# Kernel tuning notes

Hardware: AMD Instinct MI355X
Metric: run time of the kernel (lower is better)

The kernel has to match this reference:

```python
import jax, jax.numpy as jnp
import numpy as np

B, S, D, H = 4, 2048, 1024, 16  # batch, seq, n_embd, n_head
HD = D // H  # head size = 64


def setup_inputs() -> dict:
    key = jax.random.key(0)
    ks = jax.random.split(key, 5)
    s = 0.02
    return {
        "x": jax.random.normal(ks[0], (B, S, D), dtype=jnp.float32),
        "W_attn": jax.random.normal(ks[1], (D, 3 * D), dtype=jnp.float32) * s,
        "b_attn": jnp.zeros((3 * D,), dtype=jnp.float32),
        "W_proj": jax.random.normal(ks[2], (D, D), dtype=jnp.float32) * s,
        "b_proj": jnp.zeros((D,), dtype=jnp.float32),
    }


def reference(x, W_attn, b_attn, W_proj, b_proj):
    Bx, Sx, Dx = x.shape
    qkv = x @ W_attn + b_attn  # [B,S,3D]
    q, k, v = jnp.split(qkv, 3, axis=-1)
    # [B,H,S,hd]
    q = q.reshape(Bx, Sx, H, HD).transpose(0, 2, 1, 3)
    k = k.reshape(Bx, Sx, H, HD).transpose(0, 2, 1, 3)
    v = v.reshape(Bx, Sx, H, HD).transpose(0, 2, 1, 3)
    scale = 1.0 / jnp.sqrt(jnp.asarray(HD, dtype=x.dtype))
    att = jnp.einsum("bhqd,bhkd->bhqk", q, k) * scale  # [B,H,S,S]
    causal = jnp.tril(jnp.ones((Sx, Sx), dtype=bool))
    att = jnp.where(causal[None, None, :, :], att, jnp.asarray(-jnp.inf, dtype=att.dtype))
    att = jax.nn.softmax(att, axis=-1)
    y = jnp.einsum("bhqk,bhkd->bhqd", att, v)  # [B,H,S,hd]
    y = y.transpose(0, 2, 1, 3).reshape(Bx, Sx, Dx)
    return y @ W_proj + b_proj
```

## Files before the change

### kernel.cpp

```cpp
#include <hip/hip_runtime.h>
#include <math.h>

#define SEQ 2048
#define DIM 1024
#define NH 16
#define HD 64
#define QKV_LD 3072

typedef __attribute__((ext_vector_type(8))) __bf16 bf16x8;
typedef __attribute__((ext_vector_type(8))) unsigned short u16x8;
typedef __attribute__((ext_vector_type(4))) unsigned short u16x4;
typedef __attribute__((ext_vector_type(4))) float f32x4;

typedef unsigned int __attribute__((may_alias)) u32a;

__device__ __forceinline__ unsigned short f2b(float f) {
  unsigned int b = __builtin_bit_cast(unsigned int, f);
  return (unsigned short)((b + 0x7fffu + ((b >> 16) & 1u)) >> 16);
}

__device__ __forceinline__ void gload_lds16(const void* g, void* l) {
  __builtin_amdgcn_global_load_lds((const __attribute__((address_space(1))) void*)g,
                                   (__attribute__((address_space(3))) void*)l,
                                   16, 0, 0);
}

__device__ __forceinline__ bf16x8 ld_frag16(const unsigned short* p) {
  bf16x8 r;
  __builtin_memcpy(&r, __builtin_assume_aligned((void*)p, 16), 16);
  return r;
}


__global__ void to_bf16_kernel(const float* __restrict__ x,
                               unsigned short* __restrict__ y, int n) {
  int i = (blockIdx.x * blockDim.x + threadIdx.x) * 4;
  if (i >= n) return;
  float4 v = *(const float4*)(x + i);
  u16x4 o;
  o.x = f2b(v.x); o.y = f2b(v.y); o.z = f2b(v.z); o.w = f2b(v.w);
  *(u16x4*)(y + i) = o;
}

__global__ void transpose_to_bf16_kernel(const float* __restrict__ W,
                                         unsigned short* __restrict__ WT,
                                         int K, int N) {
  __shared__ float tile[32][33];
  const int n0 = blockIdx.x * 32, k0 = blockIdx.y * 32;
  const int tx = threadIdx.x, ty = threadIdx.y;
  tile[ty][tx] = W[(size_t)(k0 + ty) * N + n0 + tx];
  __syncthreads();
  WT[(size_t)(n0 + ty) * K + k0 + tx] = f2b(tile[tx][ty]);
}


template <int OUT_F32>
__global__ __launch_bounds__(256, 2) void gemm_bt_kernel(
    const unsigned short* __restrict__ A,
    const unsigned short* __restrict__ BT,
    const float* __restrict__ bias,
    void* __restrict__ C, int M, int N, int K,
    int scale_cols, float scale_val) {
  __shared__ unsigned short As[128 * 32];
  __shared__ unsigned short Bs[128 * 32];

  const int tid = threadIdx.x;
  const int wave = tid >> 6;
  const int lane = tid & 63;
  const int quad = lane >> 4;
  const int l16 = lane & 15;
  const int m0 = blockIdx.y * 128;
  const int n0 = blockIdx.x * 128;
  const int wm = (wave >> 1) * 64;
  const int wn = (wave & 1) * 64;

  const size_t a_g = (size_t)(m0 + wave * 32 + (lane >> 2)) * K + (lane & 3) * 8;
  const size_t b_g = (size_t)(n0 + wave * 32 + (lane >> 2)) * K + (lane & 3) * 8;
  unsigned short* lA = As + wave * 1024;
  unsigned short* lB = Bs + wave * 1024;

  f32x4 acc[4][4] = {};

  for (int k0 = 0; k0 < K; k0 += 32) {
    gload_lds16(A + a_g + k0, lA);
    gload_lds16(A + a_g + (size_t)16 * K + k0, lA + 512);
    gload_lds16(BT + b_g + k0, lB);
    gload_lds16(BT + b_g + (size_t)16 * K + k0, lB + 512);
    __syncthreads();

    bf16x8 af[4], bfr[4];
#pragma unroll
    for (int i = 0; i < 4; ++i)
      af[i] = *(const bf16x8*)&As[(wm + i * 16 + l16) * 32 + quad * 8];
#pragma unroll
    for (int i = 0; i < 4; ++i)
      bfr[i] = *(const bf16x8*)&Bs[(wn + i * 16 + l16) * 32 + quad * 8];
#pragma unroll
    for (int mi = 0; mi < 4; ++mi)
#pragma unroll
      for (int ni = 0; ni < 4; ++ni)
        acc[mi][ni] = __builtin_amdgcn_mfma_f32_16x16x32_bf16(af[mi], bfr[ni],
                                                              acc[mi][ni], 0, 0, 0);
    __syncthreads();
  }

#pragma unroll
  for (int mi = 0; mi < 4; ++mi) {
#pragma unroll
    for (int ni = 0; ni < 4; ++ni) {
      const int col = n0 + wn + ni * 16 + l16;
      const int row = m0 + wm + mi * 16 + quad * 4;
      const float bv = bias[col];
      const float sv = (col < scale_cols) ? scale_val : 1.0f;
#pragma unroll
      for (int r = 0; r < 4; ++r) {
        float v = (acc[mi][ni][r] + bv) * sv;
        if (OUT_F32)
          ((float*)C)[(size_t)(row + r) * N + col] = v;
        else
          ((unsigned short*)C)[(size_t)(row + r) * N + col] = f2b(v);
      }
    }
  }
}


__global__ __launch_bounds__(256, 4) void flash_kernel(
    const unsigned short* __restrict__ qkv,
    unsigned short* __restrict__ yatt) {
  __shared__ unsigned short Ks[2][2][64 * 32];
  __shared__ __align__(16) unsigned short Vt[8 * 64 * 8];
  __shared__ __align__(16) unsigned short Ps[4][16 * 72];

  const int tid = threadIdx.x;
  const int w = tid >> 6;
  const int lane = tid & 63;
  const int quad = lane >> 4;
  const int l16 = lane & 15;
  const int b = blockIdx.y >> 4;
  const int h = blockIdx.y & 15;
  const int jt = blockIdx.x;

  const unsigned short* base = qkv + (size_t)b * SEQ * QKV_LD;

  const int ktok_l = w * 16 + (lane >> 2);
  const int ksw = (ktok_l ^ (ktok_l >> 2)) & 3;
  const int kchunk = (lane & 3) ^ ksw;
  const int rsw = (l16 ^ (l16 >> 2)) & 3;

  const int vk = tid >> 3;
  const int vc = (tid & 7) * 8;

  int vwidx[8];
#pragma unroll
  for (int j = 0; j < 8; ++j)
    vwidx[j] = (vk >> 2) * 256 + (vc | ((j + (vc >> 3)) & 7)) * 4 + (vk & 3);

  int vroff[4];
#pragma unroll
  for (int ni = 0; ni < 4; ++ni) {
    const int dim = ni * 16 + l16;
    vroff[ni] = ((dim & 56) | ((dim + (dim >> 3)) & 7)) * 8;
  }

  u16x8 ob = {};
  if (l16 == 0) {
#pragma unroll
    for (int j = 0; j < 8; ++j) ob[j] = 0x3F80;
  }
  const bf16x8 onesb = __builtin_bit_cast(bf16x8, ob);

  for (int pass = 0; pass < 2; ++pass) {
    const int qt = pass == 0 ? (31 - jt) : jt;
    const int q0 = qt * 64;
    const int kt = qt + 1;

    const unsigned short* qp =
        base + (size_t)(q0 + w * 16 + l16) * QKV_LD + h * HD + quad * 8;
    const bf16x8 qf0 = *(const bf16x8*)qp;
    const bf16x8 qf1 = *(const bf16x8*)(qp + 32);

    f32x4 o[4] = {};
    f32x4 lacc = {};

    u16x8 va, vb;
    {
      const unsigned short* kg =
          base + (size_t)ktok_l * QKV_LD + DIM + h * HD + kchunk * 8;
      gload_lds16(kg, &Ks[0][0][w * 512]);
      gload_lds16(kg + 32, &Ks[0][1][w * 512]);
      const unsigned short* vg =
          base + (size_t)(2 * vk) * QKV_LD + 2 * DIM + h * HD + vc;
      va = *(const u16x8*)vg;
      vb = *(const u16x8*)(vg + QKV_LD);
    }
    __syncthreads();
    {
      u32a* V32 = (u32a*)Vt;
#pragma unroll
      for (int j = 0; j < 8; ++j)
        V32[vwidx[j]] = (unsigned int)va[j] | ((unsigned int)vb[j] << 16);
    }
    __syncthreads();

    for (int t = 0; t < kt; ++t) {
      const int cur = t & 1;
      if (t + 1 < kt) {
        const unsigned short* kg =
            base + (size_t)((t + 1) * 64 + ktok_l) * QKV_LD + DIM + h * HD + kchunk * 8;
        gload_lds16(kg, &Ks[1 - cur][0][w * 512]);
        gload_lds16(kg + 32, &Ks[1 - cur][1][w * 512]);
        const unsigned short* vg =
            base + (size_t)((t + 1) * 64 + 2 * vk) * QKV_LD + 2 * DIM + h * HD + vc;
        va = *(const u16x8*)vg;
        vb = *(const u16x8*)(vg + QKV_LD);
      }

      const bool diag = (t == kt - 1);
      const int qloc = w * 16 + quad * 4;
#pragma unroll
      for (int ni = 0; ni < 4; ++ni) {
        const int ro = (ni * 16 + l16) * 32 + ((quad ^ rsw) * 8);
        f32x4 a = {};
        a = __builtin_amdgcn_mfma_f32_16x16x32_bf16(
            qf0, *(const bf16x8*)&Ks[cur][0][ro], a, 0, 0, 0);
        a = __builtin_amdgcn_mfma_f32_16x16x32_bf16(
            qf1, *(const bf16x8*)&Ks[cur][1][ro], a, 0, 0, 0);
        const int kloc = ni * 16 + l16;
#pragma unroll
        for (int r = 0; r < 4; ++r) {
          float p = exp2f(a[r]);
          if (diag && kloc > qloc + r) p = 0.0f;
          Ps[w][(quad * 4 + r) * 72 + kloc] = f2b(p);
        }
      }

#pragma unroll
      for (int c = 0; c < 2; ++c) {
        const bf16x8 pa = ld_frag16(&Ps[w][l16 * 72 + c * 32 + quad * 8]);
#pragma unroll
        for (int ni = 0; ni < 4; ++ni) {
          const bf16x8 vbf = *(const bf16x8*)&Vt[(c * 4 + quad) * 512 + vroff[ni]];
          o[ni] = __builtin_amdgcn_mfma_f32_16x16x32_bf16(pa, vbf, o[ni], 0, 0, 0);
        }
        lacc = __builtin_amdgcn_mfma_f32_16x16x32_bf16(pa, onesb, lacc, 0, 0, 0);
      }

      __syncthreads();
      if (t + 1 < kt) {
        u32a* V32 = (u32a*)Vt;
#pragma unroll
        for (int j = 0; j < 8; ++j)
          V32[vwidx[j]] = (unsigned int)va[j] | ((unsigned int)vb[j] << 16);
      }
      __syncthreads();
    }

#pragma unroll
    for (int r = 0; r < 4; ++r) {
      const float lv = __shfl(lacc[r], quad << 4);
      const float inv = 1.0f / lv;
      const int row = q0 + w * 16 + quad * 4 + r;
      unsigned short* dst = yatt + (size_t)(b * SEQ + row) * DIM + h * HD + l16;
#pragma unroll
      for (int ni = 0; ni < 4; ++ni)
        dst[ni * 16] = f2b(o[ni][r] * inv);
    }
  }
}


extern "C" void kernel_launch(void* const* d_in, const int* in_sizes, int n_in,
                              void* d_out, int out_size, void* d_ws, size_t ws_size,
                              hipStream_t stream) {
  const float* x  = (const float*)d_in[0];
  const float* Wa = (const float*)d_in[1];
  const float* ba = (const float*)d_in[2];
  const float* Wp = (const float*)d_in[3];
  const float* bp = (const float*)d_in[4];
  float* out = (float*)d_out;

  char* ws = (char*)d_ws;
  unsigned short* xb   = (unsigned short*)ws;
  unsigned short* WaT  = (unsigned short*)(ws + 16777216);
  unsigned short* WpT  = (unsigned short*)(ws + 23068672);
  unsigned short* qkv  = (unsigned short*)(ws + 25165824);
  unsigned short* yatt = (unsigned short*)(ws + 75497472);

  const int M = 4 * SEQ;
  const float qscale = 0.125f * 1.44269504089f;

  to_bf16_kernel<<<8192, 256, 0, stream>>>(x, xb, M * DIM);
  transpose_to_bf16_kernel<<<dim3(96, 32), dim3(32, 32), 0, stream>>>(Wa, WaT, DIM, 3 * DIM);
  transpose_to_bf16_kernel<<<dim3(32, 32), dim3(32, 32), 0, stream>>>(Wp, WpT, DIM, DIM);

  gemm_bt_kernel<0><<<dim3(24, 64), 256, 0, stream>>>(xb, WaT, ba, qkv, M, 3 * DIM, DIM,
                                                      DIM, qscale);

  flash_kernel<<<dim3(16, 4 * NH), 256, 0, stream>>>(qkv, yatt);

  gemm_bt_kernel<1><<<dim3(8, 64), 256, 0, stream>>>(yatt, WpT, bp, out, M, DIM, DIM,
                                                     0, 1.0f);
}
```

Measured before the change: 283.4 us.

## Process two 64-row query tiles per flash block to reuse K/V tiles

The flash kernel now handles a 128-row query block split into two 64-row sub-tiles per pass. Each staged K/V tile is loaded into registers once and reused for both sub-tiles, with causal skipping of the upper sub-tile on the last key tile. The aim is to halve K/V global and LDS traffic per query row. In exchange it doubles accumulator registers, lowers the occupancy target to 2, and halves the grid to 512 blocks, which may hurt latency hiding and load balance.

Measured after the change: 289.9 us. 2.3% more time.

```diff
diff --git a/kernel.cpp b/kernel.cpp
--- a/kernel.cpp
+++ b/kernel.cpp
@@ -125,7 +125,7 @@
 }
 
 
-__global__ __launch_bounds__(256, 4) void flash_kernel(
+__global__ __launch_bounds__(256, 2) void flash_kernel(
     const unsigned short* __restrict__ qkv,
     unsigned short* __restrict__ yatt) {
   __shared__ unsigned short Ks[2][2][64 * 32];
@@ -171,17 +171,21 @@
   const bf16x8 onesb = __builtin_bit_cast(bf16x8, ob);
 
   for (int pass = 0; pass < 2; ++pass) {
-    const int qt = pass == 0 ? (31 - jt) : jt;
-    const int q0 = qt * 64;
-    const int kt = qt + 1;
-
-    const unsigned short* qp =
-        base + (size_t)(q0 + w * 16 + l16) * QKV_LD + h * HD + quad * 8;
-    const bf16x8 qf0 = *(const bf16x8*)qp;
-    const bf16x8 qf1 = *(const bf16x8*)(qp + 32);
-
-    f32x4 o[4] = {};
-    f32x4 lacc = {};
+    const int qt = pass == 0 ? (15 - jt) : jt;
+    const int q0 = qt * 128;
+    const int kt = 2 * qt + 2;
+
+    bf16x8 qf[2][2];
+#pragma unroll
+    for (int m = 0; m < 2; ++m) {
+      const unsigned short* qp =
+          base + (size_t)(q0 + m * 64 + w * 16 + l16) * QKV_LD + h * HD + quad * 8;
+      qf[m][0] = *(const bf16x8*)qp;
+      qf[m][1] = *(const bf16x8*)(qp + 32);
+    }
+
+    f32x4 o[2][4] = {};
+    f32x4 lacc[2] = {};
 
     u16x8 va, vb;
     {
@@ -216,34 +220,48 @@
         vb = *(const u16x8*)(vg + QKV_LD);
       }
 
-      const bool diag = (t == kt - 1);
-      const int qloc = w * 16 + quad * 4;
+      bf16x8 kf[2][4], vf[2][4];
 #pragma unroll
       for (int ni = 0; ni < 4; ++ni) {
         const int ro = (ni * 16 + l16) * 32 + ((quad ^ rsw) * 8);
-        f32x4 a = {};
-        a = __builtin_amdgcn_mfma_f32_16x16x32_bf16(
-            qf0, *(const bf16x8*)&Ks[cur][0][ro], a, 0, 0, 0);
-        a = __builtin_amdgcn_mfma_f32_16x16x32_bf16(
-            qf1, *(const bf16x8*)&Ks[cur][1][ro], a, 0, 0, 0);
-        const int kloc = ni * 16 + l16;
-#pragma unroll
-        for (int r = 0; r < 4; ++r) {
-          float p = exp2f(a[r]);
-          if (diag && kloc > qloc + r) p = 0.0f;
-          Ps[w][(quad * 4 + r) * 72 + kloc] = f2b(p);
+        kf[0][ni] = ld_frag16(&Ks[cur][0][ro]);
+        kf[1][ni] = ld_frag16(&Ks[cur][1][ro]);
+      }
+#pragma unroll
+      for (int c = 0; c < 2; ++c)
+#pragma unroll
+        for (int ni = 0; ni < 4; ++ni)
+          vf[c][ni] = ld_frag16(&Vt[(c * 4 + quad) * 512 + vroff[ni]]);
+
+      const int qloc = w * 16 + quad * 4;
+#pragma unroll
+      for (int m = 0; m < 2; ++m) {
+        if (m == 0 && t == kt - 1) continue;
+        const bool diag = (t == kt - 2 + m);
+
+#pragma unroll
+        for (int ni = 0; ni < 4; ++ni) {
+          f32x4 a = {};
+          a = __builtin_amdgcn_mfma_f32_16x16x32_bf16(qf[m][0], kf[0][ni], a, 0, 0, 0);
+          a = __builtin_amdgcn_mfma_f32_16x16x32_bf16(qf[m][1], kf[1][ni], a, 0, 0, 0);
+          const int kloc = ni * 16 + l16;
+#pragma unroll
+          for (int r = 0; r < 4; ++r) {
+            float p = exp2f(a[r]);
+            if (diag && kloc > qloc + r) p = 0.0f;
+            Ps[w][(quad * 4 + r) * 72 + kloc] = f2b(p);
+          }
         }
-      }
-
-#pragma unroll
-      for (int c = 0; c < 2; ++c) {
-        const bf16x8 pa = ld_frag16(&Ps[w][l16 * 72 + c * 32 + quad * 8]);
-#pragma unroll
-        for (int ni = 0; ni < 4; ++ni) {
-          const bf16x8 vbf = *(const bf16x8*)&Vt[(c * 4 + quad) * 512 + vroff[ni]];
-          o[ni] = __builtin_amdgcn_mfma_f32_16x16x32_bf16(pa, vbf, o[ni], 0, 0, 0);
+
+#pragma unroll
+        for (int c = 0; c < 2; ++c) {
+          const bf16x8 pa = ld_frag16(&Ps[w][l16 * 72 + c * 32 + quad * 8]);
+#pragma unroll
+          for (int ni = 0; ni < 4; ++ni)
+            o[m][ni] = __builtin_amdgcn_mfma_f32_16x16x32_bf16(pa, vf[c][ni],
+                                                               o[m][ni], 0, 0, 0);
+          lacc[m] = __builtin_amdgcn_mfma_f32_16x16x32_bf16(pa, onesb, lacc[m], 0, 0, 0);
         }
-        lacc = __builtin_amdgcn_mfma_f32_16x16x32_bf16(pa, onesb, lacc, 0, 0, 0);
       }
 
       __syncthreads();
@@ -257,14 +275,17 @@
     }
 
 #pragma unroll
-    for (int r = 0; r < 4; ++r) {
-      const float lv = __shfl(lacc[r], quad << 4);
-      const float inv = 1.0f / lv;
-      const int row = q0 + w * 16 + quad * 4 + r;
-      unsigned short* dst = yatt + (size_t)(b * SEQ + row) * DIM + h * HD + l16;
-#pragma unroll
-      for (int ni = 0; ni < 4; ++ni)
-        dst[ni * 16] = f2b(o[ni][r] * inv);
+    for (int m = 0; m < 2; ++m) {
+#pragma unroll
+      for (int r = 0; r < 4; ++r) {
+        const float lv = __shfl(lacc[m][r], quad << 4);
+        const float inv = 1.0f / lv;
+        const int row = q0 + m * 64 + w * 16 + quad * 4 + r;
+        unsigned short* dst = yatt + (size_t)(b * SEQ + row) * DIM + h * HD + l16;
+#pragma unroll
+        for (int ni = 0; ni < 4; ++ni)
+          dst[ni * 16] = f2b(o[m][ni][r] * inv);
+      }
     }
   }
 }
@@ -297,7 +318,7 @@
   gemm_bt_kernel<0><<<dim3(24, 64), 256, 0, stream>>>(xb, WaT, ba, qkv, M, 3 * DIM, DIM,
                                                       DIM, qscale);
 
-  flash_kernel<<<dim3(16, 4 * NH), 256, 0, stream>>>(qkv, yatt);
+  flash_kernel<<<dim3(8, 4 * NH), 256, 0, stream>>>(qkv, yatt);
 
   gemm_bt_kernel<1><<<dim3(8, 64), 256, 0, stream>>>(yatt, WpT, bp, out, M, DIM, DIM,
                                                      0, 1.0f);
```

## Process 128-row query blocks per K/V tile with triple-buffered continuous pipeline

Applied to the files above, without the earlier changes.

The flash kernel now gives each wave two 64-row query sub-blocks (128 rows per workgroup), so every loaded K/V tile is reused for twice as many queries. The two paired query tiles run as one continuous stream of 34 K/V tiles with a 3-deep K ring buffer, prefetch two tiles ahead, and hand-written waitcnt+barrier asm in place of __syncthreads. The grid is halved to 8x64 workgroups, launch bounds drop to 2 blocks per CU, and P is rounded to bf16 by truncation instead of round-to-nearest. In exchange it uses more registers, has fewer workgroups for load balance, and the hand-tuned vmcnt assumptions are fragile.

Result: no change. 282.4 us (-0.3%).

```diff
diff --git a/kernel.cpp b/kernel.cpp
--- a/kernel.cpp
+++ b/kernel.cpp
@@ -30,6 +30,10 @@
   __builtin_memcpy(&r, __builtin_assume_aligned((void*)p, 16), 16);
   return r;
 }
+
+#define BARRIER_VM4()  asm volatile("s_waitcnt vmcnt(4)\ns_barrier" ::: "memory")
+#define BARRIER_LGKM() asm volatile("s_waitcnt lgkmcnt(0)\ns_barrier" ::: "memory")
+#define ISSUE_FENCE()  asm volatile("" ::: "memory")
 
 
 __global__ void to_bf16_kernel(const float* __restrict__ x,
@@ -125,10 +129,93 @@
 }
 
 
-__global__ __launch_bounds__(256, 4) void flash_kernel(
+#define FA_PREFETCH(g_, via_, vib_)                                            \
+  {                                                                            \
+    const int _g = (g_);                                                       \
+    const int _tg = (_g < ktA) ? _g : ((_g < 34) ? (_g - ktA) : 0);            \
+    const unsigned short* _kg =                                                \
+        base + (size_t)(_tg * 64 + ktok_l) * QKV_LD + DIM + h * HD + kchunk * 8; \
+    gload_lds16(_kg, &Ks[_g % 3][0][w * 512]);                                 \
+    gload_lds16(_kg + 32, &Ks[_g % 3][1][w * 512]);                            \
+    const unsigned short* _vg =                                                \
+        base + (size_t)(_tg * 64 + 2 * vk) * QKV_LD + 2 * DIM + h * HD + vc;   \
+    via_ = *(const u16x8*)_vg;                                                 \
+    vib_ = *(const u16x8*)(_vg + QKV_LD);                                      \
+  }
+
+#define VT_WRITE(va_, vb_)                                                     \
+  {                                                                            \
+    u32a* _V32 = (u32a*)Vt;                                                    \
+    _Pragma("unroll") for (int j = 0; j < 8; ++j)                              \
+      _V32[vwidx[j]] = (unsigned int)(va_)[j] | ((unsigned int)(vb_)[j] << 16);\
+  }
+
+#define FA_COMPUTE(i_, t_, kt_, qf_)                                           \
+  {                                                                            \
+    const unsigned short* _kb0 = &Ks[(i_) % 3][0][0];                          \
+    const unsigned short* _kb1 = &Ks[(i_) % 3][1][0];                          \
+    bf16x8 kf0[4], kf1[4], vf0[4], vf1[4];                                     \
+    _Pragma("unroll") for (int ni = 0; ni < 4; ++ni) {                         \
+      const int ro = (ni * 16 + l16) * 32 + ((quad ^ rsw) * 8);                \
+      kf0[ni] = ld_frag16(_kb0 + ro);                                          \
+      kf1[ni] = ld_frag16(_kb1 + ro);                                          \
+      vf0[ni] = ld_frag16(&Vt[quad * 512 + vroff[ni]]);                        \
+      vf1[ni] = ld_frag16(&Vt[(4 + quad) * 512 + vroff[ni]]);                  \
+    }                                                                          \
+    const int qloc = w * 16 + quad * 4;                                        \
+    _Pragma("unroll") for (int m = 0; m < 2; ++m) {                            \
+      if (!(m == 0 && (t_) == (kt_)-1)) {   \
+        const bool diag = ((t_) == (kt_)-2 + m);                               \
+        _Pragma("unroll") for (int ni = 0; ni < 4; ++ni) {                     \
+          f32x4 a = {};                                                        \
+          a = __builtin_amdgcn_mfma_f32_16x16x32_bf16(qf_[m][0], kf0[ni], a, 0, 0, 0); \
+          a = __builtin_amdgcn_mfma_f32_16x16x32_bf16(qf_[m][1], kf1[ni], a, 0, 0, 0); \
+          const int kloc = ni * 16 + l16;                                      \
+          _Pragma("unroll") for (int r = 0; r < 4; ++r) {                      \
+            float p = exp2f(a[r]);                                             \
+            if (diag && kloc > qloc + r) p = 0.0f;                 \
+            Ps[w][(quad * 4 + r) * 72 + kloc] =                                \
+                (unsigned short)(__builtin_bit_cast(unsigned int, p) >> 16);   \
+          }                                                                    \
+        }                                                                      \
+        _Pragma("unroll") for (int c = 0; c < 2; ++c) {                        \
+          const bf16x8 pa = ld_frag16(&Ps[w][l16 * 72 + c * 32 + quad * 8]);   \
+          _Pragma("unroll") for (int ni = 0; ni < 4; ++ni)                     \
+            o[m][ni] = __builtin_amdgcn_mfma_f32_16x16x32_bf16(                \
+                pa, c ? vf1[ni] : vf0[ni], o[m][ni], 0, 0, 0);                 \
+          lacc[m] = __builtin_amdgcn_mfma_f32_16x16x32_bf16(pa, onesb,         \
+                                                            lacc[m], 0, 0, 0);\
+        }                                                                      \
+      }                                                                        \
+    }                                                                          \
+  }
+
+#define FA_ITER(i_, t_, kt_, qf_, pva, pvb, cva, cvb)                          \
+  {                                                                            \
+    FA_PREFETCH((i_) + 2, pva, pvb);                                           \
+    FA_COMPUTE(i_, t_, kt_, qf_);                                              \
+    BARRIER_VM4();                                                             \
+    if ((i_) + 1 < 34) {                                                       \
+      VT_WRITE(cva, cvb);                                                      \
+      BARRIER_LGKM();                                                          \
+    }                                                                          \
+  }
+
+#define FA_EPILOGUE(q0_)                                                       \
+  _Pragma("unroll") for (int m = 0; m < 2; ++m)                                \
+  _Pragma("unroll") for (int r = 0; r < 4; ++r) {                              \
+    const float lv = __shfl(lacc[m][r], quad << 4);                            \
+    const float inv = 1.0f / lv;                                               \
+    const int row = (q0_) + m * 64 + w * 16 + quad * 4 + r;                    \
+    unsigned short* dst = yatt + (size_t)(b * SEQ + row) * DIM + h * HD + l16; \
+    _Pragma("unroll") for (int ni = 0; ni < 4; ++ni)                           \
+      dst[ni * 16] = f2b(o[m][ni][r] * inv);                                   \
+  }
+
+__global__ __launch_bounds__(256, 2) void flash_kernel(
     const unsigned short* __restrict__ qkv,
     unsigned short* __restrict__ yatt) {
-  __shared__ unsigned short Ks[2][2][64 * 32];
+  __shared__ unsigned short Ks[3][2][64 * 32];
   __shared__ __align__(16) unsigned short Vt[8 * 64 * 8];
   __shared__ __align__(16) unsigned short Ps[4][16 * 72];
 
@@ -143,6 +230,11 @@
 
   const unsigned short* base = qkv + (size_t)b * SEQ * QKV_LD;
 
+  const int qtA = 15 - jt, qtB = jt;
+  const int ktA = 2 * qtA + 2;
+  const int ktB = 34 - ktA;
+  const int q0A = qtA * 128, q0B = qtB * 128;
+
   const int ktok_l = w * 16 + (lane >> 2);
   const int ksw = (ktok_l ^ (ktok_l >> 2)) & 3;
   const int kchunk = (lane & 3) ^ ksw;
@@ -150,12 +242,10 @@
 
   const int vk = tid >> 3;
   const int vc = (tid & 7) * 8;
-
   int vwidx[8];
 #pragma unroll
   for (int j = 0; j < 8; ++j)
     vwidx[j] = (vk >> 2) * 256 + (vc | ((j + (vc >> 3)) & 7)) * 4 + (vk & 3);
-
   int vroff[4];
 #pragma unroll
   for (int ni = 0; ni < 4; ++ni) {
@@ -170,103 +260,48 @@
   }
   const bf16x8 onesb = __builtin_bit_cast(bf16x8, ob);
 
-  for (int pass = 0; pass < 2; ++pass) {
-    const int qt = pass == 0 ? (31 - jt) : jt;
-    const int q0 = qt * 64;
-    const int kt = qt + 1;
-
-    const unsigned short* qp =
-        base + (size_t)(q0 + w * 16 + l16) * QKV_LD + h * HD + quad * 8;
-    const bf16x8 qf0 = *(const bf16x8*)qp;
-    const bf16x8 qf1 = *(const bf16x8*)(qp + 32);
-
-    f32x4 o[4] = {};
-    f32x4 lacc = {};
-
-    u16x8 va, vb;
-    {
-      const unsigned short* kg =
-          base + (size_t)ktok_l * QKV_LD + DIM + h * HD + kchunk * 8;
-      gload_lds16(kg, &Ks[0][0][w * 512]);
-      gload_lds16(kg + 32, &Ks[0][1][w * 512]);
-      const unsigned short* vg =
-          base + (size_t)(2 * vk) * QKV_LD + 2 * DIM + h * HD + vc;
-      va = *(const u16x8*)vg;
-      vb = *(const u16x8*)(vg + QKV_LD);
-    }
-    __syncthreads();
-    {
-      u32a* V32 = (u32a*)Vt;
-#pragma unroll
-      for (int j = 0; j < 8; ++j)
-        V32[vwidx[j]] = (unsigned int)va[j] | ((unsigned int)vb[j] << 16);
-    }
-    __syncthreads();
-
-    for (int t = 0; t < kt; ++t) {
-      const int cur = t & 1;
-      if (t + 1 < kt) {
-        const unsigned short* kg =
-            base + (size_t)((t + 1) * 64 + ktok_l) * QKV_LD + DIM + h * HD + kchunk * 8;
-        gload_lds16(kg, &Ks[1 - cur][0][w * 512]);
-        gload_lds16(kg + 32, &Ks[1 - cur][1][w * 512]);
-        const unsigned short* vg =
-            base + (size_t)((t + 1) * 64 + 2 * vk) * QKV_LD + 2 * DIM + h * HD + vc;
-        va = *(const u16x8*)vg;
-        vb = *(const u16x8*)(vg + QKV_LD);
-      }
-
-      const bool diag = (t == kt - 1);
-      const int qloc = w * 16 + quad * 4;
-#pragma unroll
-      for (int ni = 0; ni < 4; ++ni) {
-        const int ro = (ni * 16 + l16) * 32 + ((quad ^ rsw) * 8);
-        f32x4 a = {};
-        a = __builtin_amdgcn_mfma_f32_16x16x32_bf16(
-            qf0, *(const bf16x8*)&Ks[cur][0][ro], a, 0, 0, 0);
-        a = __builtin_amdgcn_mfma_f32_16x16x32_bf16(
-            qf1, *(const bf16x8*)&Ks[cur][1][ro], a, 0, 0, 0);
-        const int kloc = ni * 16 + l16;
-#pragma unroll
-        for (int r = 0; r < 4; ++r) {
-          float p = exp2f(a[r]);
-          if (diag && kloc > qloc + r) p = 0.0f;
-          Ps[w][(quad * 4 + r) * 72 + kloc] = f2b(p);
-        }
-      }
-
-#pragma unroll
-      for (int c = 0; c < 2; ++c) {
-        const bf16x8 pa = ld_frag16(&Ps[w][l16 * 72 + c * 32 + quad * 8]);
-#pragma unroll
-        for (int ni = 0; ni < 4; ++ni) {
-          const bf16x8 vbf = *(const bf16x8*)&Vt[(c * 4 + quad) * 512 + vroff[ni]];
-          o[ni] = __builtin_amdgcn_mfma_f32_16x16x32_bf16(pa, vbf, o[ni], 0, 0, 0);
-        }
-        lacc = __builtin_amdgcn_mfma_f32_16x16x32_bf16(pa, onesb, lacc, 0, 0, 0);
-      }
-
-      __syncthreads();
-      if (t + 1 < kt) {
-        u32a* V32 = (u32a*)Vt;
-#pragma unroll
-        for (int j = 0; j < 8; ++j)
-          V32[vwidx[j]] = (unsigned int)va[j] | ((unsigned int)vb[j] << 16);
-      }
-      __syncthreads();
-    }
-
-#pragma unroll
-    for (int r = 0; r < 4; ++r) {
-      const float lv = __shfl(lacc[r], quad << 4);
-      const float inv = 1.0f / lv;
-      const int row = q0 + w * 16 + quad * 4 + r;
-      unsigned short* dst = yatt + (size_t)(b * SEQ + row) * DIM + h * HD + l16;
-#pragma unroll
-      for (int ni = 0; ni < 4; ++ni)
-        dst[ni * 16] = f2b(o[ni][r] * inv);
-    }
-  }
+  bf16x8 qfA[2][2], qfB[2][2];
+#pragma unroll
+  for (int m = 0; m < 2; ++m) {
+    const unsigned short* qa =
+        base + (size_t)(q0A + m * 64 + w * 16 + l16) * QKV_LD + h * HD + quad * 8;
+    qfA[m][0] = *(const bf16x8*)qa;
+    qfA[m][1] = *(const bf16x8*)(qa + 32);
+    const unsigned short* qb =
+        base + (size_t)(q0B + m * 64 + w * 16 + l16) * QKV_LD + h * HD + quad * 8;
+    qfB[m][0] = *(const bf16x8*)qb;
+    qfB[m][1] = *(const bf16x8*)(qb + 32);
+  }
+
+  u16x8 va0, vb0, va1, vb1;
+  ISSUE_FENCE();
+  FA_PREFETCH(0, va0, vb0);
+  ISSUE_FENCE();
+  FA_PREFETCH(1, va1, vb1);
+  BARRIER_VM4();
+  VT_WRITE(va0, vb0);
+  BARRIER_LGKM();
+
+  f32x4 o[2][4] = {};
+  f32x4 lacc[2] = {};
+
+  for (int i = 0; i < ktA; i += 2) {
+    FA_ITER(i,     i,     ktA, qfA, va0, vb0, va1, vb1);
+    FA_ITER(i + 1, i + 1, ktA, qfA, va1, vb1, va0, vb0);
+  }
+  FA_EPILOGUE(q0A);
+#pragma unroll
+  for (int m = 0; m < 2; ++m) {
+    lacc[m] = (f32x4){};
+#pragma unroll
+    for (int ni = 0; ni < 4; ++ni) o[m][ni] = (f32x4){};
+  }
+
+  for (int i = ktA; i < 34; i += 2) {
+    FA_ITER(i,     i - ktA,     ktB, qfB, va0, vb0, va1, vb1);
+    FA_ITER(i + 1, i + 1 - ktA, ktB, qfB, va1, vb1, va0, vb0);
+  }
+  FA_EPILOGUE(q0B);
 }
 
 
@@ -297,7 +332,7 @@
   gemm_bt_kernel<0><<<dim3(24, 64), 256, 0, stream>>>(xb, WaT, ba, qkv, M, 3 * DIM, DIM,
                                                       DIM, qscale);
 
-  flash_kernel<<<dim3(16, 4 * NH), 256, 0, stream>>>(qkv, yatt);
+  flash_kernel<<<dim3(8, 4 * NH), 256, 0, stream>>>(qkv, yatt);
 
   gemm_bt_kernel<1><<<dim3(8, 64), 256, 0, stream>>>(yatt, WpT, bp, out, M, DIM, DIM,
                                                      0, 1.0f);
```
